# Performance work log

Hardware: AMD Instinct MI355X
Metric: run time of the kernel (lower is better)

Reference implementation:

```python
import jax, jax.numpy as jnp
import numpy as np
from jax import lax

B, S, D, H, L, V = 8, 512, 768, 12, 12, 40478
DH = D // H          # 64 head dim
DF = 4 * D           # 3072 ffn dim
STD = 0.02
EPS = 1e-5


def setup_inputs() -> dict:
    key = jax.random.key(0)
    ks = jax.random.split(key, 8)
    tokens = jax.random.randint(ks[0], (B, S), 0, V)
    # single embedding table: vocab rows then n_ctx positional rows (GPT style)
    we = jax.random.normal(ks[1], (V + S, D), jnp.float32) * STD
    wqkv = jax.random.normal(ks[2], (L, D, 3 * D), jnp.float32) * STD
    bqkv = jnp.zeros((L, 3 * D), jnp.float32)
    wproj = jax.random.normal(ks[3], (L, D, D), jnp.float32) * STD
    bproj = jnp.zeros((L, D), jnp.float32)
    g1 = jnp.ones((L, D), jnp.float32)
    b1 = jnp.zeros((L, D), jnp.float32)
    wfc = jax.random.normal(ks[4], (L, D, DF), jnp.float32) * STD
    bfc = jnp.zeros((L, DF), jnp.float32)
    wpr = jax.random.normal(ks[5], (L, DF, D), jnp.float32) * STD
    bpr = jnp.zeros((L, D), jnp.float32)
    g2 = jnp.ones((L, D), jnp.float32)
    b2 = jnp.zeros((L, D), jnp.float32)
    return dict(tokens=tokens, we=we, wqkv=wqkv, bqkv=bqkv, wproj=wproj,
                bproj=bproj, g1=g1, b1=b1, wfc=wfc, bfc=bfc, wpr=wpr,
                bpr=bpr, g2=g2, b2=b2)


def _ln(x, g, b):
    u = x.mean(-1, keepdims=True)
    s = ((x - u) ** 2).mean(-1, keepdims=True)
    return g * (x - u) / jnp.sqrt(s + EPS) + b


def _gelu(x):
    c = jnp.sqrt(2.0 / jnp.pi).astype(x.dtype)
    return 0.5 * x * (1.0 + jnp.tanh(c * (x + 0.044715 * x ** 3)))


def reference(tokens, we, wqkv, bqkv, wproj, bproj, g1, b1, wfc, bfc, wpr, bpr, g2, b2):
    pos_ids = V + jnp.arange(S)
    h = we[tokens] + we[pos_ids][None, :, :]          # [B,S,D]
    mask = jnp.tril(jnp.ones((S, S), h.dtype))        # causal tril buffer

    def block(x, p):
        wq, bq, wp, bp, gA, bA, wf, bf, wr, br, gB, bB = p
        qkv = x @ wq + bq                             # [B,S,3D]
        q, k, v = jnp.split(qkv, 3, axis=-1)
        def heads(t):
            return t.reshape(B, S, H, DH).transpose(0, 2, 1, 3)  # [B,H,S,DH]
        q, k, v = heads(q), heads(k), heads(v)
        w = jnp.einsum('bhqd,bhkd->bhqk', q, k) / jnp.sqrt(jnp.asarray(DH, x.dtype))
        w = w * mask + (-1e9) * (1.0 - mask)
        w = jax.nn.softmax(w, axis=-1)
        a = jnp.einsum('bhqk,bhkd->bhqd', w, v)       # [B,H,S,DH]
        a = a.transpose(0, 2, 1, 3).reshape(B, S, D)
        a = a @ wp + bp                               # attn output proj
        n = _ln(x + a, gA, bA)
        m = (_gelu(n @ wf + bf)) @ wr + br            # GELU MLP
        return _ln(n + m, gB, bB), None

    h, _ = lax.scan(block, h, (wqkv, bqkv, wproj, bproj, g1, b1,
                               wfc, bfc, wpr, bpr, g2, b2))
    return h
```

## Files before the change

kernel.cpp:

```cpp
#include <hip/hip_runtime.h>
#include <math.h>

#define BB 8
#define SS 512
#define DD 768
#define HH 12
#define LL 12
#define DFF 3072
#define VV 40478
#define MM (BB*SS)

typedef _Float16 half8 __attribute__((ext_vector_type(8)));
typedef _Float16 half4 __attribute__((ext_vector_type(4)));
typedef float floatx4 __attribute__((ext_vector_type(4)));

#define GLDS(gptr, lptr) \
    __builtin_amdgcn_global_load_lds( \
        (const __attribute__((address_space(1))) void*)(gptr), \
        (__attribute__((address_space(3))) void*)(lptr), 16, 0, 0)

__global__ __launch_bounds__(256) void embed_kernel(
    const int* __restrict__ tokens, const float* __restrict__ we,
    float* __restrict__ x, _Float16* __restrict__ x16)
{
    int i = blockIdx.x;
    int s = i & (SS - 1);
    int tok = tokens[i];
    const float* wt = we + (size_t)tok * DD;
    const float* wp = we + (size_t)(VV + s) * DD;
    float* xr = x + (size_t)i * DD;
    _Float16* hr = x16 + (size_t)i * DD;
    for (int d = threadIdx.x; d < DD; d += 256) {
        float v = wt[d] + wp[d];
        xr[d] = v;
        hr[d] = (_Float16)v;
    }
}

__global__ __launch_bounds__(256) void convw_kernel(
    const float* __restrict__ W, _Float16* __restrict__ Wt, int K, int N)
{
    __shared__ float tile[64][65];
    const int n0 = blockIdx.x * 64, k0 = blockIdx.y * 64;
    const int t = threadIdx.x;
    const int c  = t & 63;
    const int r4 = t >> 6;
#pragma unroll
    for (int rr = 0; rr < 64; rr += 4)
        tile[rr + r4][c] = W[(size_t)(k0 + rr + r4) * N + n0 + c];
    __syncthreads();
#pragma unroll
    for (int nn = 0; nn < 64; nn += 4) {
        int n = nn + r4;
        Wt[(size_t)(n0 + n) * K + k0 + c] = (_Float16)tile[c][n];
    }
}

#define EPI_BIAS_RES 1
#define EPI_BIAS_GELU 2
#define EPI_QKV 3

template<int EPI>
__global__ __launch_bounds__(256) void gemm_h_kernel(
    const _Float16* __restrict__ A, const _Float16* __restrict__ Bt,
    const float* __restrict__ bias, const float* __restrict__ resid,
    float* __restrict__ C, _Float16* __restrict__ h16o,
    _Float16* __restrict__ k16o, _Float16* __restrict__ vTo,
    int M, int N, int K)
{
    __shared__ _Float16 As[4096];
    __shared__ _Float16 Bs[4096];

    const int tid  = threadIdx.x;
    const int lane = tid & 63;
    const int wave = tid >> 6;
    const int row0 = blockIdx.y * 128, col0 = blockIdx.x * 128;

    const int srow = ((tid >> 6) << 4) + (tid & 15);
    const int skc  = (tid >> 4) & 3;
    const _Float16* aptr0 = A  + (size_t)(row0 + srow) * K      + skc * 8;
    const _Float16* aptr1 = A  + (size_t)(row0 + 64 + srow) * K + skc * 8;
    const _Float16* bptr0 = Bt + (size_t)(col0 + srow) * K      + skc * 8;
    const _Float16* bptr1 = Bt + (size_t)(col0 + 64 + srow) * K + skc * 8;

    const int wm = (wave >> 1) << 2;
    const int wn = (wave & 1) << 2;

    floatx4 acc[4][4] = {};

    for (int kk = 0; kk < K; kk += 32) {
        __syncthreads();
        GLDS(aptr0, As + tid * 8);
        GLDS(aptr1, As + 2048 + tid * 8);
        GLDS(bptr0, Bs + tid * 8);
        GLDS(bptr1, Bs + 2048 + tid * 8);
        aptr0 += 32; aptr1 += 32; bptr0 += 32; bptr1 += 32;
        __syncthreads();

        half8 af[4], bf[4];
#pragma unroll
        for (int i = 0; i < 4; ++i) af[i] = *(const half8*)&As[((wm + i) * 64 + lane) * 8];
#pragma unroll
        for (int i = 0; i < 4; ++i) bf[i] = *(const half8*)&Bs[((wn + i) * 64 + lane) * 8];
#pragma unroll
        for (int i = 0; i < 4; ++i)
#pragma unroll
            for (int j = 0; j < 4; ++j)
                acc[i][j] = __builtin_amdgcn_mfma_f32_16x16x32_f16(
                    af[i], bf[j], acc[i][j], 0, 0, 0);
    }

    if (EPI == EPI_QKV) {
        const int part = col0 / 768;
#pragma unroll
        for (int i = 0; i < 4; ++i) {
            int rowb = row0 + ((wm + i) << 4) + ((lane >> 4) << 2);
            int bidx = rowb >> 9;
            int s0   = rowb & 511;
#pragma unroll
            for (int j = 0; j < 4; ++j) {
                int col = col0 + ((wn + j) << 4) + (lane & 15);
                float bsv = bias[col];
                int hh = (col >> 6) % 12;
                int dd = col & 63;
                size_t hb = ((size_t)(bidx * 12 + hh)) << 15;
                if (part == 0) {
#pragma unroll
                    for (int r = 0; r < 4; ++r)
                        h16o[hb + (size_t)(s0 + r) * 64 + dd] =
                            (_Float16)((acc[i][j][r] + bsv) * 0.125f);
                } else if (part == 1) {
#pragma unroll
                    for (int r = 0; r < 4; ++r)
                        k16o[hb + (size_t)(s0 + r) * 64 + dd] =
                            (_Float16)(acc[i][j][r] + bsv);
                } else {
                    half4 pk;
#pragma unroll
                    for (int r = 0; r < 4; ++r)
                        pk[r] = (_Float16)(acc[i][j][r] + bsv);
                    *(half4*)&vTo[hb + (size_t)dd * 512 + s0] = pk;
                }
            }
        }
    } else {
#pragma unroll
        for (int i = 0; i < 4; ++i) {
            int rowb = row0 + ((wm + i) << 4) + ((lane >> 4) << 2);
#pragma unroll
            for (int j = 0; j < 4; ++j) {
                int col = col0 + ((wn + j) << 4) + (lane & 15);
                float bsv = bias[col];
#pragma unroll
                for (int r = 0; r < 4; ++r) {
                    int row = rowb + r;
                    float v = acc[i][j][r] + bsv;
                    if (EPI == EPI_BIAS_RES) {
                        v += resid[(size_t)row * N + col];
                        C[(size_t)row * N + col] = v;
                    }
                    if (EPI == EPI_BIAS_GELU) {
                        float u = v;
                        v = 0.5f * u * (1.0f + tanhf(0.7978845608028654f * (u + 0.044715f * u * u * u)));
                        h16o[(size_t)row * N + col] = (_Float16)v;
                    }
                }
            }
        }
    }
}

__global__ __launch_bounds__(256) void attn_kernel(
    const _Float16* __restrict__ q16, const _Float16* __restrict__ k16,
    const _Float16* __restrict__ vT16, _Float16* __restrict__ attnb)
{
    const int qt = 7 - blockIdx.x;
    const int h  = blockIdx.y;
    const int b  = blockIdx.z;
    const int tid  = threadIdx.x;
    const int lane = tid & 63;
    const int wave = tid >> 6;
    const int quad = lane >> 4;
    const int l15  = lane & 15;
    const int wq   = wave << 4;

    __shared__ _Float16 Kt[64 * 72];
    __shared__ _Float16 Vt[64 * 72];
    __shared__ _Float16 Ps[64 * 72];
    __shared__ float    Ss[64 * 68];
    __shared__ float mS[64], lS[64], aS[64];

    const size_t headbase = ((size_t)(b * HH + h)) << 15;
    const int q0 = qt * 64;

    half8 qf0, qf1;
    {
        const _Float16* qp = q16 + headbase + (size_t)(q0 + wq + l15) * 64 + quad * 8;
        qf0 = *(const half8*)qp;
        qf1 = *(const half8*)(qp + 32);
    }
    if (tid < 64) { mS[tid] = -1e30f; lS[tid] = 0.f; }

    floatx4 o[4] = {};

    for (int kt = 0; kt <= qt; ++kt) {
        {
            int r = tid >> 2;
            int c = (tid & 3) << 4;
            const _Float16* kp = k16 + headbase + (size_t)(kt * 64 + r) * 64 + c;
            half8 k0 = *(const half8*)kp;
            half8 k1 = *(const half8*)(kp + 8);
            const _Float16* vp = vT16 + headbase + (size_t)r * 512 + kt * 64 + c;
            half8 v0 = *(const half8*)vp;
            half8 v1 = *(const half8*)(vp + 8);
            __syncthreads();
            *(half8*)&Kt[r * 72 + c]     = k0;
            *(half8*)&Kt[r * 72 + c + 8] = k1;
            *(half8*)&Vt[r * 72 + c]     = v0;
            *(half8*)&Vt[r * 72 + c + 8] = v1;
        }
        __syncthreads();

        floatx4 s4[4];
#pragma unroll
        for (int t4 = 0; t4 < 4; ++t4) {
            half8 kf0 = *(const half8*)&Kt[(t4 * 16 + l15) * 72 + quad * 8];
            half8 kf1 = *(const half8*)&Kt[(t4 * 16 + l15) * 72 + quad * 8 + 32];
            floatx4 a = {};
            a = __builtin_amdgcn_mfma_f32_16x16x32_f16(qf0, kf0, a, 0, 0, 0);
            a = __builtin_amdgcn_mfma_f32_16x16x32_f16(qf1, kf1, a, 0, 0, 0);
            s4[t4] = a;
        }

        if (kt == qt) {
#pragma unroll
            for (int t4 = 0; t4 < 4; ++t4) {
                int kc = t4 * 16 + l15;
#pragma unroll
                for (int r = 0; r < 4; ++r)
                    if (kc > wq + quad * 4 + r) s4[t4][r] = -1e30f;
            }
        }

#pragma unroll
        for (int t4 = 0; t4 < 4; ++t4)
#pragma unroll
            for (int r = 0; r < 4; ++r)
                Ss[(wq + quad * 4 + r) * 68 + t4 * 16 + l15] = s4[t4][r];
        __syncthreads();

        {
            int rr = tid >> 2, sub = tid & 3;
            float4 p0 = *(const float4*)&Ss[rr * 68 + sub * 16 + 0];
            float4 p1 = *(const float4*)&Ss[rr * 68 + sub * 16 + 4];
            float4 p2 = *(const float4*)&Ss[rr * 68 + sub * 16 + 8];
            float4 p3 = *(const float4*)&Ss[rr * 68 + sub * 16 + 12];
            float tmax = fmaxf(fmaxf(fmaxf(p0.x, p0.y), fmaxf(p0.z, p0.w)),
                         fmaxf(fmaxf(fmaxf(p1.x, p1.y), fmaxf(p1.z, p1.w)),
                         fmaxf(fmaxf(fmaxf(p2.x, p2.y), fmaxf(p2.z, p2.w)),
                               fmaxf(fmaxf(p3.x, p3.y), fmaxf(p3.z, p3.w)))));
            tmax = fmaxf(tmax, __shfl_xor(tmax, 1));
            tmax = fmaxf(tmax, __shfl_xor(tmax, 2));
            float mold = mS[rr];
            float mnew = fmaxf(mold, tmax);
            p0.x = __expf(p0.x - mnew); p0.y = __expf(p0.y - mnew);
            p0.z = __expf(p0.z - mnew); p0.w = __expf(p0.w - mnew);
            p1.x = __expf(p1.x - mnew); p1.y = __expf(p1.y - mnew);
            p1.z = __expf(p1.z - mnew); p1.w = __expf(p1.w - mnew);
            p2.x = __expf(p2.x - mnew); p2.y = __expf(p2.y - mnew);
            p2.z = __expf(p2.z - mnew); p2.w = __expf(p2.w - mnew);
            p3.x = __expf(p3.x - mnew); p3.y = __expf(p3.y - mnew);
            p3.z = __expf(p3.z - mnew); p3.w = __expf(p3.w - mnew);
            float sum = p0.x + p0.y + p0.z + p0.w + p1.x + p1.y + p1.z + p1.w
                      + p2.x + p2.y + p2.z + p2.w + p3.x + p3.y + p3.z + p3.w;
            sum += __shfl_xor(sum, 1);
            sum += __shfl_xor(sum, 2);
            half8 ph0, ph1;
            ph0[0] = (_Float16)p0.x; ph0[1] = (_Float16)p0.y;
            ph0[2] = (_Float16)p0.z; ph0[3] = (_Float16)p0.w;
            ph0[4] = (_Float16)p1.x; ph0[5] = (_Float16)p1.y;
            ph0[6] = (_Float16)p1.z; ph0[7] = (_Float16)p1.w;
            ph1[0] = (_Float16)p2.x; ph1[1] = (_Float16)p2.y;
            ph1[2] = (_Float16)p2.z; ph1[3] = (_Float16)p2.w;
            ph1[4] = (_Float16)p3.x; ph1[5] = (_Float16)p3.y;
            ph1[6] = (_Float16)p3.z; ph1[7] = (_Float16)p3.w;
            *(half8*)&Ps[rr * 72 + sub * 16]     = ph0;
            *(half8*)&Ps[rr * 72 + sub * 16 + 8] = ph1;
            if (sub == 0) {
                float al = __expf(mold - mnew);
                aS[rr] = al;
                mS[rr] = mnew;
                lS[rr] = lS[rr] * al + sum;
            }
        }
        __syncthreads();

        {
            float al[4];
#pragma unroll
            for (int r = 0; r < 4; ++r) al[r] = aS[wq + quad * 4 + r];
#pragma unroll
            for (int dt = 0; dt < 4; ++dt)
#pragma unroll
                for (int r = 0; r < 4; ++r) o[dt][r] *= al[r];

            half8 pf0 = *(const half8*)&Ps[(wq + l15) * 72 + quad * 8];
            half8 pf1 = *(const half8*)&Ps[(wq + l15) * 72 + quad * 8 + 32];
#pragma unroll
            for (int dt = 0; dt < 4; ++dt) {
                half8 vf0 = *(const half8*)&Vt[(dt * 16 + l15) * 72 + quad * 8];
                half8 vf1 = *(const half8*)&Vt[(dt * 16 + l15) * 72 + quad * 8 + 32];
                o[dt] = __builtin_amdgcn_mfma_f32_16x16x32_f16(pf0, vf0, o[dt], 0, 0, 0);
                o[dt] = __builtin_amdgcn_mfma_f32_16x16x32_f16(pf1, vf1, o[dt], 0, 0, 0);
            }
        }
    }

    float inv[4];
#pragma unroll
    for (int r = 0; r < 4; ++r) inv[r] = 1.0f / lS[wq + quad * 4 + r];
#pragma unroll
    for (int dt = 0; dt < 4; ++dt) {
        int col = h * 64 + dt * 16 + l15;
#pragma unroll
        for (int r = 0; r < 4; ++r) {
            int row = b * SS + q0 + wq + quad * 4 + r;
            attnb[(size_t)row * DD + col] = (_Float16)(o[dt][r] * inv[r]);
        }
    }
}

__global__ __launch_bounds__(256) void ln_kernel(
    const float* __restrict__ in, const float* __restrict__ gam,
    const float* __restrict__ bet, float* __restrict__ out,
    _Float16* __restrict__ out16)
{
    int row = blockIdx.x;
    int tid = threadIdx.x;
    const float* p = in + (size_t)row * DD;
    float v0 = p[tid], v1 = p[tid + 256], v2 = p[tid + 512];

    __shared__ float red[256];
    red[tid] = v0 + v1 + v2;
    __syncthreads();
    for (int off = 128; off > 0; off >>= 1) {
        if (tid < off) red[tid] += red[tid + off];
        __syncthreads();
    }
    float mean = red[0] * (1.0f / DD);
    __syncthreads();

    float d0 = v0 - mean, d1 = v1 - mean, d2 = v2 - mean;
    red[tid] = d0 * d0 + d1 * d1 + d2 * d2;
    __syncthreads();
    for (int off = 128; off > 0; off >>= 1) {
        if (tid < off) red[tid] += red[tid + off];
        __syncthreads();
    }
    float rstd = rsqrtf(red[0] * (1.0f / DD) + 1e-5f);

    float* o = out + (size_t)row * DD;
    float r0 = gam[tid]       * (d0 * rstd) + bet[tid];
    float r1 = gam[tid + 256] * (d1 * rstd) + bet[tid + 256];
    float r2 = gam[tid + 512] * (d2 * rstd) + bet[tid + 512];
    o[tid] = r0; o[tid + 256] = r1; o[tid + 512] = r2;
    if (out16) {
        _Float16* oh = out16 + (size_t)row * DD;
        oh[tid] = (_Float16)r0; oh[tid + 256] = (_Float16)r1; oh[tid + 512] = (_Float16)r2;
    }
}

extern "C" void kernel_launch(void* const* d_in, const int* in_sizes, int n_in,
                              void* d_out, int out_size, void* d_ws, size_t ws_size,
                              hipStream_t stream)
{
    const int*   tokens = (const int*)d_in[0];
    const float* we     = (const float*)d_in[1];
    const float* wqkv   = (const float*)d_in[2];
    const float* bqkv   = (const float*)d_in[3];
    const float* wproj  = (const float*)d_in[4];
    const float* bproj  = (const float*)d_in[5];
    const float* g1     = (const float*)d_in[6];
    const float* b1     = (const float*)d_in[7];
    const float* wfc    = (const float*)d_in[8];
    const float* bfc    = (const float*)d_in[9];
    const float* wpr    = (const float*)d_in[10];
    const float* bpr    = (const float*)d_in[11];
    const float* g2     = (const float*)d_in[12];
    const float* b2     = (const float*)d_in[13];
    float* out = (float*)d_out;

    float* x   = (float*)d_ws;
    float* n   = x + (size_t)MM * DD;
    _Float16* x16  = (_Float16*)(n + (size_t)MM * DD);
    _Float16* n16  = x16 + (size_t)MM * DD;
    _Float16* WBUF = n16 + (size_t)MM * DD;
    _Float16* BIG  = WBUF + (size_t)DD * DFF;
    _Float16* q16  = BIG;
    _Float16* k16  = q16 + (size_t)MM * DD;
    _Float16* vT16 = k16 + (size_t)MM * DD;
    _Float16* attnb16 = vT16 + (size_t)MM * DD;
    float*    t   = (float*)BIG;
    _Float16* m16 = BIG;

    embed_kernel<<<dim3(MM), 256, 0, stream>>>(tokens, we, x, x16);

    for (int l = 0; l < LL; ++l) {
        convw_kernel<<<dim3(2304 / 64, DD / 64), 256, 0, stream>>>(
            wqkv + (size_t)l * DD * 2304, WBUF, DD, 2304);
        gemm_h_kernel<EPI_QKV><<<dim3(2304 / 128, MM / 128), 256, 0, stream>>>(
            x16, WBUF, bqkv + (size_t)l * 2304, nullptr, nullptr,
            q16, k16, vT16, MM, 2304, DD);
        attn_kernel<<<dim3(SS / 64, HH, BB), 256, 0, stream>>>(q16, k16, vT16, attnb16);
        convw_kernel<<<dim3(DD / 64, DD / 64), 256, 0, stream>>>(
            wproj + (size_t)l * DD * DD, WBUF, DD, DD);
        gemm_h_kernel<EPI_BIAS_RES><<<dim3(DD / 128, MM / 128), 256, 0, stream>>>(
            attnb16, WBUF, bproj + (size_t)l * DD,
            x, t, nullptr, nullptr, nullptr, MM, DD, DD);
        ln_kernel<<<dim3(MM), 256, 0, stream>>>(t, g1 + (size_t)l * DD,
                                                b1 + (size_t)l * DD, n, n16);
        convw_kernel<<<dim3(DFF / 64, DD / 64), 256, 0, stream>>>(
            wfc + (size_t)l * DD * DFF, WBUF, DD, DFF);
        gemm_h_kernel<EPI_BIAS_GELU><<<dim3(DFF / 128, MM / 128), 256, 0, stream>>>(
            n16, WBUF, bfc + (size_t)l * DFF, nullptr, nullptr,
            m16, nullptr, nullptr, MM, DFF, DD);
        convw_kernel<<<dim3(DD / 64, DFF / 64), 256, 0, stream>>>(
            wpr + (size_t)l * DFF * DD, WBUF, DFF, DD);
        gemm_h_kernel<EPI_BIAS_RES><<<dim3(DD / 128, MM / 128), 256, 0, stream>>>(
            m16, WBUF, bpr + (size_t)l * DD,
            n, x, nullptr, nullptr, nullptr, MM, DD, DFF);
        ln_kernel<<<dim3(MM), 256, 0, stream>>>(x, g2 + (size_t)l * DD,
                                                b2 + (size_t)l * DD,
                                                (l == LL - 1) ? out : x,
                                                (l == LL - 1) ? nullptr : x16);
    }
}
```

Before: 3.550 ms.

## Double-buffer GEMM LDS loads, swizzle block order, batch weight conversions

The GEMM main loop now uses two LDS buffers so the global-to-LDS loads for the next K step are issued before the MFMAs on the current step, with explicit vmcnt waits and barriers in place of two syncthreads per iteration. Block indices are remapped with an 8-way swizzle to change which tiles run together and improve L2 reuse. Three of the four per-layer weight transposes are merged into one launch writing separate buffers, which cuts launch count. LDS use per block doubles, which may lower occupancy, and the swizzle assumes the block count divides by 8.

```diff
diff --git a/kernel.cpp b/kernel.cpp
--- a/kernel.cpp
+++ b/kernel.cpp
@@ -37,11 +37,11 @@
     }
 }
 
-__global__ __launch_bounds__(256) void convw_kernel(
-    const float* __restrict__ W, _Float16* __restrict__ Wt, int K, int N)
+__device__ __forceinline__ void convw_tile(
+    const float* __restrict__ W, _Float16* __restrict__ Wt,
+    int K, int N, int n0, int k0)
 {
     __shared__ float tile[64][65];
-    const int n0 = blockIdx.x * 64, k0 = blockIdx.y * 64;
     const int t = threadIdx.x;
     const int c  = t & 63;
     const int r4 = t >> 6;
@@ -54,6 +54,29 @@
         int n = nn + r4;
         Wt[(size_t)(n0 + n) * K + k0 + c] = (_Float16)tile[c][n];
     }
+}
+
+__global__ __launch_bounds__(256) void convw_kernel(
+    const float* __restrict__ W, _Float16* __restrict__ Wt, int K, int N)
+{
+    const int ntx = N >> 6;
+    const int b = blockIdx.x;
+    convw_tile(W, Wt, K, N, (b % ntx) * 64, (b / ntx) * 64);
+}
+
+__global__ __launch_bounds__(256) void convw3_kernel(
+    const float* __restrict__ w0, const float* __restrict__ w1,
+    const float* __restrict__ w2,
+    _Float16* __restrict__ o0, _Float16* __restrict__ o1,
+    _Float16* __restrict__ o2)
+{
+    int b = blockIdx.x;
+    const float* W; _Float16* Wt; int N, tb;
+    if (b < 432)       { W = w0; Wt = o0; N = 2304; tb = b; }
+    else if (b < 576)  { W = w1; Wt = o1; N = 768;  tb = b - 432; }
+    else               { W = w2; Wt = o2; N = 3072; tb = b - 576; }
+    const int ntx = N >> 6;
+    convw_tile(W, Wt, 768, N, (tb % ntx) * 64, (tb / ntx) * 64);
 }
 
 #define EPI_BIAS_RES 1
@@ -68,13 +91,18 @@
     _Float16* __restrict__ k16o, _Float16* __restrict__ vTo,
     int M, int N, int K)
 {
-    __shared__ _Float16 As[4096];
-    __shared__ _Float16 Bs[4096];
+    __shared__ _Float16 As[2][4096];
+    __shared__ _Float16 Bs[2][4096];
 
     const int tid  = threadIdx.x;
     const int lane = tid & 63;
     const int wave = tid >> 6;
-    const int row0 = blockIdx.y * 128, col0 = blockIdx.x * 128;
+
+    const int gx  = gridDim.x;
+    const int lb  = blockIdx.y * gx + blockIdx.x;
+    const int q8  = (gx * gridDim.y) >> 3;
+    const int swz = (lb & 7) * q8 + (lb >> 3);
+    const int row0 = (swz / gx) * 128, col0 = (swz % gx) * 128;
 
     const int srow = ((tid >> 6) << 4) + (tid & 15);
     const int skc  = (tid >> 4) & 3;
@@ -88,26 +116,46 @@
 
     floatx4 acc[4][4] = {};
 
-    for (int kk = 0; kk < K; kk += 32) {
-        __syncthreads();
-        GLDS(aptr0, As + tid * 8);
-        GLDS(aptr1, As + 2048 + tid * 8);
-        GLDS(bptr0, Bs + tid * 8);
-        GLDS(bptr1, Bs + 2048 + tid * 8);
-        aptr0 += 32; aptr1 += 32; bptr0 += 32; bptr1 += 32;
-        __syncthreads();
+    const int nk = K >> 5;
+
+    GLDS(aptr0, &As[0][tid * 8]);
+    GLDS(aptr1, &As[0][2048 + tid * 8]);
+    GLDS(bptr0, &Bs[0][tid * 8]);
+    GLDS(bptr1, &Bs[0][2048 + tid * 8]);
+    aptr0 += 32; aptr1 += 32; bptr0 += 32; bptr1 += 32;
+
+    for (int t = 0; t < nk; ++t) {
+        const _Float16* Asc = As[t & 1];
+        const _Float16* Bsc = Bs[t & 1];
+        if (t + 1 < nk) {
+            _Float16* Asn = As[(t + 1) & 1];
+            _Float16* Bsn = Bs[(t + 1) & 1];
+            GLDS(aptr0, Asn + tid * 8);
+            GLDS(aptr1, Asn + 2048 + tid * 8);
+            GLDS(bptr0, Bsn + tid * 8);
+            GLDS(bptr1, Bsn + 2048 + tid * 8);
+            aptr0 += 32; aptr1 += 32; bptr0 += 32; bptr1 += 32;
+            asm volatile("s_waitcnt vmcnt(4)" ::: "memory");
+        } else {
+            asm volatile("s_waitcnt vmcnt(0)" ::: "memory");
+        }
+        __builtin_amdgcn_s_barrier();
+        asm volatile("" ::: "memory");
 
         half8 af[4], bf[4];
 #pragma unroll
-        for (int i = 0; i < 4; ++i) af[i] = *(const half8*)&As[((wm + i) * 64 + lane) * 8];
-#pragma unroll
-        for (int i = 0; i < 4; ++i) bf[i] = *(const half8*)&Bs[((wn + i) * 64 + lane) * 8];
+        for (int i = 0; i < 4; ++i) af[i] = *(const half8*)&Asc[((wm + i) * 64 + lane) * 8];
+#pragma unroll
+        for (int i = 0; i < 4; ++i) bf[i] = *(const half8*)&Bsc[((wn + i) * 64 + lane) * 8];
 #pragma unroll
         for (int i = 0; i < 4; ++i)
 #pragma unroll
             for (int j = 0; j < 4; ++j)
                 acc[i][j] = __builtin_amdgcn_mfma_f32_16x16x32_f16(
                     af[i], bf[j], acc[i][j], 0, 0, 0);
+
+        asm volatile("" ::: "memory");
+        __builtin_amdgcn_s_barrier();
     }
 
     if (EPI == EPI_QKV) {
@@ -395,7 +443,11 @@
     _Float16* x16  = (_Float16*)(n + (size_t)MM * DD);
     _Float16* n16  = x16 + (size_t)MM * DD;
     _Float16* WBUF = n16 + (size_t)MM * DD;
-    _Float16* BIG  = WBUF + (size_t)DD * DFF;
+    _Float16* wq_t = WBUF;
+    _Float16* wp_t = wq_t + (size_t)2304 * DD;
+    _Float16* wf_t = wp_t + (size_t)DD * DD;
+    _Float16* wr_t = WBUF;
+    _Float16* BIG  = wf_t + (size_t)DFF * DD;
     _Float16* q16  = BIG;
     _Float16* k16  = q16 + (size_t)MM * DD;
     _Float16* vT16 = k16 + (size_t)MM * DD;
@@ -406,28 +458,25 @@
     embed_kernel<<<dim3(MM), 256, 0, stream>>>(tokens, we, x, x16);
 
     for (int l = 0; l < LL; ++l) {
-        convw_kernel<<<dim3(2304 / 64, DD / 64), 256, 0, stream>>>(
-            wqkv + (size_t)l * DD * 2304, WBUF, DD, 2304);
+        convw3_kernel<<<dim3(1152), 256, 0, stream>>>(
+            wqkv + (size_t)l * DD * 2304, wproj + (size_t)l * DD * DD,
+            wfc + (size_t)l * DD * DFF, wq_t, wp_t, wf_t);
         gemm_h_kernel<EPI_QKV><<<dim3(2304 / 128, MM / 128), 256, 0, stream>>>(
-            x16, WBUF, bqkv + (size_t)l * 2304, nullptr, nullptr,
+            x16, wq_t, bqkv + (size_t)l * 2304, nullptr, nullptr,
             q16, k16, vT16, MM, 2304, DD);
         attn_kernel<<<dim3(SS / 64, HH, BB), 256, 0, stream>>>(q16, k16, vT16, attnb16);
-        convw_kernel<<<dim3(DD / 64, DD / 64), 256, 0, stream>>>(
-            wproj + (size_t)l * DD * DD, WBUF, DD, DD);
         gemm_h_kernel<EPI_BIAS_RES><<<dim3(DD / 128, MM / 128), 256, 0, stream>>>(
-            attnb16, WBUF, bproj + (size_t)l * DD,
+            attnb16, wp_t, bproj + (size_t)l * DD,
             x, t, nullptr, nullptr, nullptr, MM, DD, DD);
         ln_kernel<<<dim3(MM), 256, 0, stream>>>(t, g1 + (size_t)l * DD,
                                                 b1 + (size_t)l * DD, n, n16);
-        convw_kernel<<<dim3(DFF / 64, DD / 64), 256, 0, stream>>>(
-            wfc + (size_t)l * DD * DFF, WBUF, DD, DFF);
         gemm_h_kernel<EPI_BIAS_GELU><<<dim3(DFF / 128, MM / 128), 256, 0, stream>>>(
-            n16, WBUF, bfc + (size_t)l * DFF, nullptr, nullptr,
+            n16, wf_t, bfc + (size_t)l * DFF, nullptr, nullptr,
             m16, nullptr, nullptr, MM, DFF, DD);
-        convw_kernel<<<dim3(DD / 64, DFF / 64), 256, 0, stream>>>(
-            wpr + (size_t)l * DFF * DD, WBUF, DFF, DD);
+        convw_kernel<<<dim3(576), 256, 0, stream>>>(
+            wpr + (size_t)l * DFF * DD, wr_t, DFF, DD);
         gemm_h_kernel<EPI_BIAS_RES><<<dim3(DD / 128, MM / 128), 256, 0, stream>>>(
-            m16, WBUF, bpr + (size_t)l * DD,
+            m16, wr_t, bpr + (size_t)l * DD,
             n, x, nullptr, nullptr, nullptr, MM, DD, DFF);
         ln_kernel<<<dim3(MM), 256, 0, stream>>>(x, g2 + (size_t)l * DD,
                                                 b2 + (size_t)l * DD,
```

Measured after the change: 3.301 ms. -7.0%, faster.
